# Optimization experiments

Hardware: AMD Instinct MI355X
Metric: run time of the kernel (lower is better)

The kernel has to match this reference:

```python
import jax, jax.numpy as jnp
import numpy as np

E = 8          # num_experts
R = 16         # lora rank
TOP_K = 2
SCALING = 32.0 / 16.0   # lora_alpha / r
D_IN = 4096
D_OUT = 4096


def setup_inputs() -> dict:
    key = jax.random.key(0)
    ks = jax.random.split(key, 6)
    x = jax.random.normal(ks[0], (4, 2048, D_IN), jnp.float32)
    Wb = jax.random.normal(ks[1], (D_OUT, D_IN), jnp.float32) * 0.02
    bias = jax.random.normal(ks[2], (D_OUT,), jnp.float32) * 0.02
    Wr = jax.random.normal(ks[3], (E, D_IN), jnp.float32) * 0.01  # router (normal init, std=0.01)
    A = jax.random.normal(ks[4], (E, R, D_IN), jnp.float32) * (1.0 / np.sqrt(D_IN))  # kaiming-ish
    Bm = jax.random.normal(ks[5], (E, D_OUT, R), jnp.float32) * 0.01  # nonzero for nontrivial baseline
    return {"x": x, "Wb": Wb, "bias": bias, "Wr": Wr, "A": A, "Bm": Bm}


def reference(x, Wb, bias, Wr, A, Bm):
    # x: [B, S, D_IN]
    xf = x.reshape(-1, x.shape[-1])                       # [T, D_IN]
    T = xf.shape[0]

    # Router: softmax -> top-k -> renormalize selected probs
    logits = xf @ Wr.T                                    # [T, E]
    probs = jax.nn.softmax(logits, axis=-1)
    topk_p, topk_i = jax.lax.top_k(probs, TOP_K)          # [T, K]
    topk_p = topk_p / jnp.sum(topk_p, axis=-1, keepdims=True)

    # Dense per-token expert weights via scatter-add (equivalent to masked dispatch/combine)
    w = jnp.zeros((T, E), xf.dtype).at[jnp.arange(T)[:, None], topk_i].add(topk_p)  # [T, E]

    # LoRA: x @ A_e^T @ B_e^T, weighted combine (dropout = identity, p=0)
    h = jnp.einsum('ti,eri->ter', xf, A)                  # [T, E, R] (small: rank-16)
    lora = jnp.einsum('ter,te,eor->to', h, w, Bm) * SCALING  # [T, D_OUT]

    base = xf @ Wb.T + bias                               # [T, D_OUT]
    out = (base + lora).reshape(*x.shape[:-1], D_OUT)
    return out
```

## Files before the change

kernel.cpp:

```cpp
#include <hip/hip_runtime.h>
#include <cmath>

typedef unsigned short ushort_t;
typedef __attribute__((ext_vector_type(8))) short short8;
typedef __attribute__((ext_vector_type(4))) float f32x4;

#define D_IN   4096
#define D_OUT  4096
#define T_TOK  8192
#define E_EXP  8
#define R_RANK 16
#define KCAT   4224
#define SCALE_LORA 2.0f

__device__ __forceinline__ ushort_t f2bf(float f) {
    unsigned int u = __float_as_uint(f);
    u += 0x7fffu + ((u >> 16) & 1u);
    return (ushort_t)(u >> 16);
}

__global__ __launch_bounds__(256) void build_weights(
    const float* __restrict__ Wb, const float* __restrict__ Bm,
    const float* __restrict__ A, ushort_t* __restrict__ Wcat,
    ushort_t* __restrict__ Abf) {
    int b = blockIdx.x;
    int tid = threadIdx.x;
    if (b < D_OUT) {
        const float4* src = (const float4*)(Wb + (size_t)b * D_IN);
        ushort_t* drow = Wcat + (size_t)b * KCAT;
        for (int c4 = tid; c4 < D_IN / 4; c4 += 256) {
            float4 v = src[c4];
            ushort4 o;
            o.x = f2bf(v.x); o.y = f2bf(v.y); o.z = f2bf(v.z); o.w = f2bf(v.w);
            ((ushort4*)drow)[c4] = o;
        }
        if (tid < E_EXP * R_RANK) {
            int e = tid >> 4, r = tid & 15;
            drow[D_IN + tid] = f2bf(Bm[((size_t)e * D_OUT + b) * R_RANK + r]);
        }
    } else {
        int er = b - D_OUT;
        const float4* src = (const float4*)(A + (size_t)er * D_IN);
        ushort_t* drow = Abf + (size_t)er * D_IN;
        for (int c4 = tid; c4 < D_IN / 4; c4 += 256) {
            float4 v = src[c4];
            ushort4 o;
            o.x = f2bf(v.x); o.y = f2bf(v.y); o.z = f2bf(v.z); o.w = f2bf(v.w);
            ((ushort4*)drow)[c4] = o;
        }
    }
}

__global__ __launch_bounds__(256) void router_convert(
    const float* __restrict__ x, const float* __restrict__ Wr,
    ushort_t* __restrict__ xcat, int2* __restrict__ eids,
    float2* __restrict__ wts) {
    __shared__ float sWr[4 * D_IN];
    int tid = threadIdx.x;
    int lane = tid & 63;
    int wave = tid >> 6;
    int tbase = blockIdx.x * 16 + wave * 4;

    float acc[4][E_EXP];
#pragma unroll
    for (int tk = 0; tk < 4; tk++)
#pragma unroll
        for (int e = 0; e < E_EXP; e++) acc[tk][e] = 0.f;

#pragma unroll
    for (int half = 0; half < 2; half++) {
        __syncthreads();
        {
            const float4* wsrc = (const float4*)(Wr + (size_t)half * 4 * D_IN);
            float4* wdst = (float4*)sWr;
#pragma unroll
            for (int q = 0; q < 16; q++)
                wdst[tid + q * 256] = wsrc[tid + q * 256];
        }
        __syncthreads();

        for (int c4 = lane; c4 < D_IN / 4; c4 += 64) {
            float4 wv[4];
#pragma unroll
            for (int e4 = 0; e4 < 4; e4++)
                wv[e4] = ((const float4*)(sWr + (size_t)e4 * D_IN))[c4];
#pragma unroll
            for (int tk = 0; tk < 4; tk++) {
                int t = tbase + tk;
                float4 v = ((const float4*)(x + (size_t)t * D_IN))[c4];
                if (half == 0) {
                    ushort4 o;
                    o.x = f2bf(v.x); o.y = f2bf(v.y); o.z = f2bf(v.z); o.w = f2bf(v.w);
                    ((ushort4*)(xcat + (size_t)t * KCAT))[c4] = o;
                }
#pragma unroll
                for (int e4 = 0; e4 < 4; e4++)
                    acc[tk][half * 4 + e4] +=
                        v.x * wv[e4].x + v.y * wv[e4].y + v.z * wv[e4].z + v.w * wv[e4].w;
            }
        }
    }

#pragma unroll
    for (int tk = 0; tk < 4; tk++)
#pragma unroll
        for (int e = 0; e < E_EXP; e++) {
#pragma unroll
            for (int off = 32; off > 0; off >>= 1)
                acc[tk][e] += __shfl_xor(acc[tk][e], off, 64);
        }
    if (lane == 0) {
#pragma unroll
        for (int tk = 0; tk < 4; tk++) {
            int t = tbase + tk;
            int e0 = 0; float l0 = acc[tk][0];
#pragma unroll
            for (int e = 1; e < E_EXP; e++)
                if (acc[tk][e] > l0) { l0 = acc[tk][e]; e0 = e; }
            int e1 = -1; float l1 = -3.4e38f;
#pragma unroll
            for (int e = 0; e < E_EXP; e++)
                if (e != e0 && acc[tk][e] > l1) { l1 = acc[tk][e]; e1 = e; }
            float w0 = 1.f / (1.f + expf(l1 - l0));
            eids[t] = make_int2(e0, e1);
            wts[t] = make_float2(w0, 1.f - w0);
        }
    }
}

__global__ __launch_bounds__(256) void h_gemm_v(
    const ushort_t* __restrict__ Abf, const int2* __restrict__ eids,
    const float2* __restrict__ wts, ushort_t* __restrict__ xcat) {
    __shared__ __align__(16) ushort_t lA[32 * 64];
    __shared__ __align__(16) ushort_t lB[128 * 64];
    int tid = threadIdx.x;
    int lane = tid & 63, wave = tid >> 6;
    int rowBase = blockIdx.x * 32;
    const ushort_t* gA = xcat + (size_t)rowBase * KCAT;

    int rA = tid >> 3;
    int kk = (tid & 7) * 8;
    ushort_t* dA = lA + (size_t)wave * 512;

    f32x4 acc[2][2];
#pragma unroll
    for (int i = 0; i < 2; i++)
#pragma unroll
        for (int j = 0; j < 2; j++)
            acc[i][j] = (f32x4){0.f, 0.f, 0.f, 0.f};

    int n0 = wave * 32;
    int row16 = lane & 15, q8 = (lane >> 4) * 8;

    for (int kt = 0; kt < D_IN; kt += 64) {
        __syncthreads();
        __builtin_amdgcn_global_load_lds(
            (const __attribute__((address_space(1))) unsigned int*)(gA + (size_t)rA * KCAT + kt + kk),
            (__attribute__((address_space(3))) unsigned int*)dA, 16, 0, 0);
#pragma unroll
        for (int q = 0; q < 4; q++) {
            __builtin_amdgcn_global_load_lds(
                (const __attribute__((address_space(1))) unsigned int*)(
                    Abf + (size_t)((tid >> 3) + 32 * q) * D_IN + kt + kk),
                (__attribute__((address_space(3))) unsigned int*)(
                    lB + (size_t)q * 2048 + (size_t)wave * 512), 16, 0, 0);
        }
        __syncthreads();

        short8 af[2][2], bfrag[2][2];
#pragma unroll
        for (int i = 0; i < 2; i++)
#pragma unroll
            for (int kc = 0; kc < 2; kc++)
                af[i][kc] = *(const short8*)&lA[(i * 16 + row16) * 64 + kc * 32 + q8];
#pragma unroll
        for (int j = 0; j < 2; j++)
#pragma unroll
            for (int kc = 0; kc < 2; kc++)
                bfrag[j][kc] = *(const short8*)&lB[(n0 + j * 16 + row16) * 64 + kc * 32 + q8];
#pragma unroll
        for (int i = 0; i < 2; i++)
#pragma unroll
            for (int j = 0; j < 2; j++) {
                acc[i][j] = __builtin_amdgcn_mfma_f32_16x16x32_bf16(
                    af[i][0], bfrag[j][0], acc[i][j], 0, 0, 0);
                acc[i][j] = __builtin_amdgcn_mfma_f32_16x16x32_bf16(
                    af[i][1], bfrag[j][1], acc[i][j], 0, 0, 0);
            }
    }

#pragma unroll
    for (int i = 0; i < 2; i++) {
        int rbase = rowBase + i * 16 + (lane >> 4) * 4;
#pragma unroll
        for (int reg = 0; reg < 4; reg++) {
            int t = rbase + reg;
            int2 e = eids[t];
            float2 w = wts[t];
#pragma unroll
            for (int j = 0; j < 2; j++) {
                int c = n0 + j * 16 + (lane & 15);
                int ce = c >> 4;
                float coef = (ce == e.x) ? (SCALE_LORA * w.x)
                           : ((ce == e.y) ? (SCALE_LORA * w.y) : 0.f);
                xcat[(size_t)t * KCAT + D_IN + c] = f2bf(coef * acc[i][j][reg]);
            }
        }
    }
}

#define GRID_M (T_TOK / 128)
#define GRID_N (D_OUT / 128)

__global__ __launch_bounds__(256) void gemm_bt_main(
    const ushort_t* __restrict__ Am, const ushort_t* __restrict__ Bmat,
    float* __restrict__ C, const float* __restrict__ bias) {
    __shared__ __align__(16) ushort_t lA[128 * 32];
    __shared__ __align__(16) ushort_t lB[128 * 32];
    const int K = KCAT, lda = KCAT, ldb = KCAT, ldc = D_OUT;
    int tid = threadIdx.x;
    int lane = tid & 63, wave = tid >> 6;

    int bid = blockIdx.x;
    int band = bid >> 8;
    int idx = bid & 255;
    const int rowBase = ((band << 3) + (idx & 7)) * 128;
    const int colBase = (idx >> 3) * 128;

    const ushort_t* gA = Am + (size_t)rowBase * lda;
    const ushort_t* gB = Bmat + (size_t)colBase * ldb;

    int c0 = tid, c1 = tid + 256;
    int r0 = c0 >> 2, k0 = (c0 & 3) * 8;
    int r1 = c1 >> 2, k1 = (c1 & 3) * 8;
    ushort_t* lA0 = lA + (size_t)wave * 512;
    ushort_t* lA1 = lA + 2048 + (size_t)wave * 512;
    ushort_t* lB0 = lB + (size_t)wave * 512;
    ushort_t* lB1 = lB + 2048 + (size_t)wave * 512;

    f32x4 acc[4][4];
#pragma unroll
    for (int i = 0; i < 4; i++)
#pragma unroll
        for (int j = 0; j < 4; j++)
            acc[i][j] = (f32x4){0.f, 0.f, 0.f, 0.f};

    int m0 = (wave >> 1) * 64, n0 = (wave & 1) * 64;
    int row16 = lane & 15, q8 = (lane >> 4) * 8;

    for (int kt = 0; kt < K; kt += 32) {
        __syncthreads();
        __builtin_amdgcn_global_load_lds(
            (const __attribute__((address_space(1))) unsigned int*)(gA + (size_t)r0 * lda + kt + k0),
            (__attribute__((address_space(3))) unsigned int*)lA0, 16, 0, 0);
        __builtin_amdgcn_global_load_lds(
            (const __attribute__((address_space(1))) unsigned int*)(gA + (size_t)r1 * lda + kt + k1),
            (__attribute__((address_space(3))) unsigned int*)lA1, 16, 0, 0);
        __builtin_amdgcn_global_load_lds(
            (const __attribute__((address_space(1))) unsigned int*)(gB + (size_t)r0 * ldb + kt + k0),
            (__attribute__((address_space(3))) unsigned int*)lB0, 16, 0, 0);
        __builtin_amdgcn_global_load_lds(
            (const __attribute__((address_space(1))) unsigned int*)(gB + (size_t)r1 * ldb + kt + k1),
            (__attribute__((address_space(3))) unsigned int*)lB1, 16, 0, 0);
        __syncthreads();

        short8 af[4], bfr[4];
#pragma unroll
        for (int i = 0; i < 4; i++)
            af[i] = *(const short8*)&lA[(m0 + i * 16 + row16) * 32 + q8];
#pragma unroll
        for (int j = 0; j < 4; j++)
            bfr[j] = *(const short8*)&lB[(n0 + j * 16 + row16) * 32 + q8];
#pragma unroll
        for (int i = 0; i < 4; i++)
#pragma unroll
            for (int j = 0; j < 4; j++)
                acc[i][j] = __builtin_amdgcn_mfma_f32_16x16x32_bf16(
                    af[i], bfr[j], acc[i][j], 0, 0, 0);
    }

#pragma unroll
    for (int i = 0; i < 4; i++) {
        int r = rowBase + m0 + i * 16 + (lane >> 4) * 4;
#pragma unroll
        for (int j = 0; j < 4; j++) {
            int cidx = colBase + n0 + j * 16 + (lane & 15);
            float badd = bias[cidx];
#pragma unroll
            for (int reg = 0; reg < 4; reg++)
                C[(size_t)(r + reg) * ldc + cidx] = acc[i][j][reg] + badd;
        }
    }
}

extern "C" void kernel_launch(void* const* d_in, const int* in_sizes, int n_in,
                              void* d_out, int out_size, void* d_ws, size_t ws_size,
                              hipStream_t stream) {
    const float* x    = (const float*)d_in[0];
    const float* Wb   = (const float*)d_in[1];
    const float* bias = (const float*)d_in[2];
    const float* Wr   = (const float*)d_in[3];
    const float* A    = (const float*)d_in[4];
    const float* Bm   = (const float*)d_in[5];
    float* out = (float*)d_out;

    char* p = (char*)d_ws;
    ushort_t* xcat = (ushort_t*)p; p += (size_t)T_TOK * KCAT * 2;
    ushort_t* Wcat = (ushort_t*)p; p += (size_t)D_OUT * KCAT * 2;
    ushort_t* Abf  = (ushort_t*)p; p += (size_t)(E_EXP * R_RANK) * D_IN * 2;
    int2*     eids = (int2*)p;     p += (size_t)T_TOK * sizeof(int2);
    float2*   wts  = (float2*)p;   p += (size_t)T_TOK * sizeof(float2);

    build_weights<<<D_OUT + E_EXP * R_RANK, 256, 0, stream>>>(Wb, Bm, A, Wcat, Abf);
    router_convert<<<T_TOK / 16, 256, 0, stream>>>(x, Wr, xcat, eids, wts);
    h_gemm_v<<<T_TOK / 32, 256, 0, stream>>>(Abf, eids, wts, xcat);
    gemm_bt_main<<<GRID_M * GRID_N, 256, 0, stream>>>(xcat, Wcat, out, bias);
}
```

Baseline: 686.0 us.

## Rewrite main GEMM with 256x256 tiles, double-buffered LDS and swizzled loads

Replaces the main bf16 GEMM's 128x128 tile, single-buffer K=32 loop with 256x256 tiles using 512 threads. The K step is now 64 and LDS is double-buffered, with a fine-grained schedule that interleaves global-to-LDS staging with MFMA phases. It also adds an XOR swizzle to avoid LDS bank conflicts, raises wave priority around MFMA bursts, and remaps blocks for L2 locality. The aim is to hide global load latency and raise arithmetic intensity per loaded byte. The costs are higher register and LDS pressure (128KB of LDS), and a hand-managed waitcnt/barrier schedule that could be fragile.

Measured after the change: 585.7 us. 14.6% less time.

```diff
diff --git a/kernel.cpp b/kernel.cpp
--- a/kernel.cpp
+++ b/kernel.cpp
@@ -209,86 +209,161 @@
     }
 }
 
-#define GRID_M (T_TOK / 128)
-#define GRID_N (D_OUT / 128)
-
-__global__ __launch_bounds__(256) void gemm_bt_main(
+#define NKT 66
+#define NIT 33
+
+__global__ __launch_bounds__(512, 2) void gemm_bt_main(
     const ushort_t* __restrict__ Am, const ushort_t* __restrict__ Bmat,
     float* __restrict__ C, const float* __restrict__ bias) {
-    __shared__ __align__(16) ushort_t lA[128 * 32];
-    __shared__ __align__(16) ushort_t lB[128 * 32];
-    const int K = KCAT, lda = KCAT, ldb = KCAT, ldc = D_OUT;
+    __shared__ __align__(16) ushort_t lds[2][2][2][128][64];
+    const int lda = KCAT, ldb = KCAT, ldc = D_OUT;
     int tid = threadIdx.x;
     int lane = tid & 63, wave = tid >> 6;
-
-    int bid = blockIdx.x;
-    int band = bid >> 8;
-    int idx = bid & 255;
-    const int rowBase = ((band << 3) + (idx & 7)) * 128;
-    const int colBase = (idx >> 3) * 128;
+    int wm = wave >> 2, wn = wave & 3;
+
+    int id = ((blockIdx.x & 7) << 6) | (blockIdx.x >> 3);
+    int band = id >> 6, wi = id & 63;
+    int mt = ((band >> 1) << 3) | (wi & 7);
+    int nt = ((band & 1) << 3) | (wi >> 3);
+    const int rowBase = mt * 256, colBase = nt * 256;
 
     const ushort_t* gA = Am + (size_t)rowBase * lda;
     const ushort_t* gB = Bmat + (size_t)colBase * ldb;
 
-    int c0 = tid, c1 = tid + 256;
-    int r0 = c0 >> 2, k0 = (c0 & 3) * 8;
-    int r1 = c1 >> 2, k1 = (c1 & 3) * 8;
-    ushort_t* lA0 = lA + (size_t)wave * 512;
-    ushort_t* lA1 = lA + 2048 + (size_t)wave * 512;
-    ushort_t* lB0 = lB + (size_t)wave * 512;
-    ushort_t* lB1 = lB + 2048 + (size_t)wave * 512;
-
-    f32x4 acc[4][4];
-#pragma unroll
-    for (int i = 0; i < 4; i++)
-#pragma unroll
-        for (int j = 0; j < 4; j++)
-            acc[i][j] = (f32x4){0.f, 0.f, 0.f, 0.f};
-
-    int m0 = (wave >> 1) * 64, n0 = (wave & 1) * 64;
-    int row16 = lane & 15, q8 = (lane >> 4) * 8;
-
-    for (int kt = 0; kt < K; kt += 32) {
-        __syncthreads();
-        __builtin_amdgcn_global_load_lds(
-            (const __attribute__((address_space(1))) unsigned int*)(gA + (size_t)r0 * lda + kt + k0),
-            (__attribute__((address_space(3))) unsigned int*)lA0, 16, 0, 0);
-        __builtin_amdgcn_global_load_lds(
-            (const __attribute__((address_space(1))) unsigned int*)(gA + (size_t)r1 * lda + kt + k1),
-            (__attribute__((address_space(3))) unsigned int*)lA1, 16, 0, 0);
-        __builtin_amdgcn_global_load_lds(
-            (const __attribute__((address_space(1))) unsigned int*)(gB + (size_t)r0 * ldb + kt + k0),
-            (__attribute__((address_space(3))) unsigned int*)lB0, 16, 0, 0);
-        __builtin_amdgcn_global_load_lds(
-            (const __attribute__((address_space(1))) unsigned int*)(gB + (size_t)r1 * ldb + kt + k1),
-            (__attribute__((address_space(3))) unsigned int*)lB1, 16, 0, 0);
-        __syncthreads();
-
-        short8 af[4], bfr[4];
-#pragma unroll
-        for (int i = 0; i < 4; i++)
-            af[i] = *(const short8*)&lA[(m0 + i * 16 + row16) * 32 + q8];
-#pragma unroll
-        for (int j = 0; j < 4; j++)
-            bfr[j] = *(const short8*)&lB[(n0 + j * 16 + row16) * 32 + q8];
-#pragma unroll
-        for (int i = 0; i < 4; i++)
-#pragma unroll
-            for (int j = 0; j < 4; j++)
-                acc[i][j] = __builtin_amdgcn_mfma_f32_16x16x32_bf16(
-                    af[i], bfr[j], acc[i][j], 0, 0, 0);
-    }
-
-#pragma unroll
-    for (int i = 0; i < 4; i++) {
-        int r = rowBase + m0 + i * 16 + (lane >> 4) * 4;
-#pragma unroll
-        for (int j = 0; j < 4; j++) {
-            int cidx = colBase + n0 + j * 16 + (lane & 15);
-            float badd = bias[cidx];
+    const int srow = tid >> 3;
+    const int scol = (((tid & 7) ^ (srow & 7)) << 3);
+
+#define STAGE(MAT, SRC, LD, BUF, KT)                                           \
+    {                                                                          \
+        _Pragma("unroll")                                                      \
+        for (int h = 0; h < 2; h++) {                                          \
+            _Pragma("unroll")                                                  \
+            for (int q = 0; q < 2; q++) {                                      \
+                __builtin_amdgcn_global_load_lds(                              \
+                    (const __attribute__((address_space(1))) unsigned int*)(   \
+                        (SRC) + (size_t)(h * 128 + q * 64 + srow) * (LD) +     \
+                        (KT) + scol),                                          \
+                    (__attribute__((address_space(3))) unsigned int*)(         \
+                        &lds[BUF][MAT][h][0][0] + q * 4096 + wave * 512),      \
+                    16, 0, 0);                                                 \
+            }                                                                  \
+        }                                                                      \
+    }
+
+    int cSwz[2];
+#pragma unroll
+    for (int kc = 0; kc < 2; kc++)
+        cSwz[kc] = (kc * 64 + (lane >> 4) * 16) ^ ((lane & 7) << 4);
+    const int rOff = (lane & 15) * 128;
+    const int bRow = (wn & 1) * 64 * 128;
+
+    const char* baseA = (const char*)&lds[0][0][wm][0][0];
+    const char* baseB = (const char*)&lds[0][1][wn >> 1][0][0];
+
+    f32x4 acc[8][4];
+#pragma unroll
+    for (int i = 0; i < 8; i++)
+#pragma unroll
+        for (int j = 0; j < 4; j++) acc[i][j] = (f32x4){0.f, 0.f, 0.f, 0.f};
+
+    short8 aF[4][2], bF[2][2];
+
+#define READ_A(BUF, S)                                                         \
+    _Pragma("unroll")                                                          \
+    for (int m4 = 0; m4 < 4; m4++) {                                           \
+        _Pragma("unroll")                                                      \
+        for (int kc = 0; kc < 2; kc++)                                         \
+            aF[m4][kc] = *(const short8*)(baseA + (BUF) * 65536 +              \
+                ((S) * 4 + m4) * 2048 + rOff + cSwz[kc]);                      \
+    }
+
+#define READ_B(BUF, U)                                                         \
+    _Pragma("unroll")                                                          \
+    for (int n2 = 0; n2 < 2; n2++) {                                           \
+        _Pragma("unroll")                                                      \
+        for (int kc = 0; kc < 2; kc++)                                         \
+            bF[n2][kc] = *(const short8*)(baseB + (BUF) * 65536 + bRow +       \
+                ((U) * 2 + n2) * 2048 + rOff + cSwz[kc]);                      \
+    }
+
+#define MFMA16(S, U)                                                           \
+    __builtin_amdgcn_s_setprio(1);                                             \
+    _Pragma("unroll")                                                          \
+    for (int m4 = 0; m4 < 4; m4++) {                                           \
+        _Pragma("unroll")                                                      \
+        for (int n2 = 0; n2 < 2; n2++) {                                       \
+            _Pragma("unroll")                                                  \
+            for (int kc = 0; kc < 2; kc++)                                     \
+                acc[(S) * 4 + m4][(U) * 2 + n2] =                              \
+                    __builtin_amdgcn_mfma_f32_16x16x32_bf16(                   \
+                        aF[m4][kc], bF[n2][kc],                                \
+                        acc[(S) * 4 + m4][(U) * 2 + n2], 0, 0, 0);             \
+        }                                                                      \
+    }                                                                          \
+    __builtin_amdgcn_s_setprio(0);
+
+#define MIDBAR()                                                               \
+    __builtin_amdgcn_s_barrier();                                              \
+    asm volatile("s_waitcnt lgkmcnt(0)" ::: "memory");
+
+#define ENDBAR() __builtin_amdgcn_s_barrier();
+
+    STAGE(0, gA, lda, 0, 0)
+    STAGE(1, gB, ldb, 0, 0)
+    STAGE(0, gA, lda, 1, 64)
+    asm volatile("s_waitcnt vmcnt(4)" ::: "memory");
+    __builtin_amdgcn_s_barrier();
+
+    for (int it = 0; it < NIT; ++it) {
+        int ktB1 = (2 * it + 1) * 64;
+        int t2 = 2 * it + 2; if (t2 > NKT - 1) t2 = NKT - 1;
+        int t3 = 2 * it + 3; if (t3 > NKT - 1) t3 = NKT - 1;
+        int kt2 = t2 * 64, kt3 = t3 * 64;
+
+        READ_A(0, 0) READ_B(0, 0)
+        STAGE(1, gB, ldb, 1, ktB1)
+        MIDBAR() MFMA16(0, 0) ENDBAR()
+
+        READ_B(0, 1)
+        MIDBAR() MFMA16(0, 1) ENDBAR()
+
+        READ_A(0, 1)
+        MIDBAR() MFMA16(1, 1) ENDBAR()
+
+        READ_B(0, 0)
+        STAGE(0, gA, lda, 0, kt2)
+        MIDBAR() MFMA16(1, 0)
+        asm volatile("s_waitcnt vmcnt(4)" ::: "memory");
+        ENDBAR()
+
+        READ_A(1, 0) READ_B(1, 0)
+        STAGE(1, gB, ldb, 0, kt2)
+        MIDBAR() MFMA16(0, 0) ENDBAR()
+
+        READ_B(1, 1)
+        MIDBAR() MFMA16(0, 1) ENDBAR()
+
+        READ_A(1, 1)
+        MIDBAR() MFMA16(1, 1) ENDBAR()
+
+        READ_B(1, 0)
+        STAGE(0, gA, lda, 1, kt3)
+        MIDBAR() MFMA16(1, 0)
+        asm volatile("s_waitcnt vmcnt(4)" ::: "memory");
+        ENDBAR()
+    }
+
+    int r0 = rowBase + wm * 128 + (lane >> 4) * 4;
+    int c0 = colBase + wn * 64 + (lane & 15);
+#pragma unroll
+    for (int mf = 0; mf < 8; mf++) {
+#pragma unroll
+        for (int nf = 0; nf < 4; nf++) {
+            int cc = c0 + nf * 16;
+            float badd = bias[cc];
 #pragma unroll
             for (int reg = 0; reg < 4; reg++)
-                C[(size_t)(r + reg) * ldc + cidx] = acc[i][j][reg] + badd;
+                C[(size_t)(r0 + mf * 16 + reg) * ldc + cc] = acc[mf][nf][reg] + badd;
         }
     }
 }
@@ -314,5 +389,5 @@
     build_weights<<<D_OUT + E_EXP * R_RANK, 256, 0, stream>>>(Wb, Bm, A, Wcat, Abf);
     router_convert<<<T_TOK / 16, 256, 0, stream>>>(x, Wr, xcat, eids, wts);
     h_gemm_v<<<T_TOK / 32, 256, 0, stream>>>(Abf, eids, wts, xcat);
-    gemm_bt_main<<<GRID_M * GRID_N, 256, 0, stream>>>(xcat, Wcat, out, bias);
-}
+    gemm_bt_main<<<(T_TOK / 256) * (D_OUT / 256), 512, 0, stream>>>(xcat, Wcat, out, bias);
+}
```
